# Kernel tuning notes

Hardware: AMD Instinct MI355X
Metric: run time of the kernel (lower is better)

## Reference

```python
import jax, jax.numpy as jnp
import numpy as np

N_NODES = 50000
N_EDGES = 800000
D_FEAT = 96
HOP_NUM = 4


def setup_inputs() -> dict:
    key = jax.random.key(0)
    k1, k2, k3, k4, k5 = jax.random.split(key, 5)
    h = jax.random.normal(k1, (N_NODES, D_FEAT), dtype=jnp.float32)
    # per-node degree-normalization scalar (ndata['d']), e.g. deg^{-1/2}
    d = jax.random.uniform(k2, (N_NODES,), dtype=jnp.float32)
    src = jax.random.randint(k3, (N_EDGES,), 0, N_NODES)
    dst = jax.random.randint(k4, (N_EDGES,), 0, N_NODES)
    # layerRegular: hop_num learned scalars, init U[0,1)
    layer_regular = jax.random.uniform(k5, (HOP_NUM,), dtype=jnp.float32)
    return {"h": h, "d": d, "src": src, "dst": dst, "layer_regular": layer_regular}


def reference(h, d, src, dst, layer_regular):
    # edge weights: e = d_dst * d_src  (edge_applying with m == 1)
    e = (d[dst] * d[src])[:, None]  # [E, 1]

    def spmm(x):
        # update_all(u_mul_e('h','e'), sum): gather src feats, scale, scatter-add to dst
        return jax.ops.segment_sum(x[src] * e, dst, num_segments=N_NODES)

    feat = h
    hops = []
    for i in range(HOP_NUM):
        r = layer_regular[i]
        feat = spmm(feat) * r + (1.0 - r) * feat  # residual blend
        # feature_drop with p=0.0 is identity
        hops.append(feat)
    return jnp.concatenate(hops, axis=1)  # [N, hop_num * D]
```

## Files before the change

### kernel.cpp

```cpp
#include <hip/hip_runtime.h>

#define N_NODES 50000
#define N_EDGES 800000
#define D_FEAT 96
#define HOP_NUM 4
#define OUT_STRIDE (HOP_NUM * D_FEAT)
#define SCAN_B 256
#define NBLK_SCAN ((N_NODES + SCAN_B - 1) / SCAN_B)
#define EB_BLOCKS ((N_EDGES + 255) / 256)
#define F2B_VEC (N_NODES * D_FEAT / 4)
#define F2B_BLOCKS ((F2B_VEC + 255) / 256)

struct Edge { int s; float w; };
typedef float f32x4 __attribute__((ext_vector_type(4)));

__device__ __forceinline__ unsigned short f2bf(float x) {
    union { float f; unsigned u; } c; c.f = x;
    unsigned r = (c.u + 0x7FFFu + ((c.u >> 16) & 1u)) >> 16;
    return (unsigned short)r;
}
__device__ __forceinline__ float bf2f(unsigned short b) {
    union { unsigned u; float f; } c; c.u = ((unsigned)b) << 16;
    return c.f;
}


__global__ void zero_deg_kernel(int* __restrict__ deg) {
    int i = blockIdx.x * blockDim.x + threadIdx.x;
    if (i < N_NODES) deg[i] = 0;
}

__global__ void hist_kernel(const int* __restrict__ dst, int* __restrict__ deg) {
    int e = blockIdx.x * blockDim.x + threadIdx.x;
    if (e >= N_EDGES) return;
    atomicAdd(&deg[dst[e]], 1);
}

__global__ void scanA_kernel(const int* __restrict__ deg, int* __restrict__ off,
                             int* __restrict__ partials, int* __restrict__ cursor) {
    int i = blockIdx.x * SCAN_B + threadIdx.x;
    int v = (i < N_NODES) ? deg[i] : 0;
    int lane = threadIdx.x & 63;
    int wid  = threadIdx.x >> 6;
    int x = v;
    #pragma unroll
    for (int o = 1; o < 64; o <<= 1) {
        int y = __shfl_up(x, o, 64);
        if (lane >= o) x += y;
    }
    __shared__ int wtot[SCAN_B / 64];
    if (lane == 63) wtot[wid] = x;
    __syncthreads();
    int wbase = 0;
    #pragma unroll
    for (int w = 0; w < SCAN_B / 64; ++w) wbase += (w < wid) ? wtot[w] : 0;
    if (i < N_NODES) {
        off[i] = wbase + x - v;
        cursor[i] = 0;
    }
    if (i == N_NODES - 1) off[N_NODES] = wbase + x;
    if (threadIdx.x == SCAN_B - 1) partials[blockIdx.x] = wbase + x;
}

__global__ void scanB_kernel(int* __restrict__ partials) {
    int tid = threadIdx.x;
    int v = (tid < NBLK_SCAN) ? partials[tid] : 0;
    int lane = tid & 63;
    int wid  = tid >> 6;
    int x = v;
    #pragma unroll
    for (int o = 1; o < 64; o <<= 1) {
        int y = __shfl_up(x, o, 64);
        if (lane >= o) x += y;
    }
    __shared__ int wtot[SCAN_B / 64];
    if (lane == 63) wtot[wid] = x;
    __syncthreads();
    int wbase = 0;
    #pragma unroll
    for (int w = 0; w < SCAN_B / 64; ++w) wbase += (w < wid) ? wtot[w] : 0;
    if (tid < NBLK_SCAN) partials[tid] = wbase + x - v;
}

__global__ void scatter_f2bf_kernel(const int* __restrict__ src, const int* __restrict__ dst,
                                    const float* __restrict__ dn,
                                    const int* __restrict__ off, const int* __restrict__ partials,
                                    int* __restrict__ cursor, Edge* __restrict__ edges,
                                    const float* __restrict__ h, unsigned short* __restrict__ tab) {
    int b = blockIdx.x;
    if (b < EB_BLOCKS) {
        int e = b * 256 + threadIdx.x;
        if (e >= N_EDGES) return;
        int t = dst[e];
        int s = src[e];
        float w = dn[s] * dn[t];
        int p = atomicAdd(&cursor[t], 1);
        int idx = off[t] + partials[t >> 8] + p;
        Edge ed; ed.s = s; ed.w = w;
        edges[idx] = ed;
    } else {
        int i = (b - EB_BLOCKS) * 256 + threadIdx.x;
        if (i >= F2B_VEC) return;
        float4 v = ((const float4*)h)[i];
        ushort4 o;
        o.x = f2bf(v.x); o.y = f2bf(v.y); o.z = f2bf(v.z); o.w = f2bf(v.w);
        ((ushort4*)tab)[i] = o;
    }
}

__global__ void spmm_gather_kernel(const unsigned short* __restrict__ tab,
                                   const int* __restrict__ off,
                                   const int* __restrict__ partials,
                                   const Edge* __restrict__ edges,
                                   const float* __restrict__ lr, int hop,
                                   float* __restrict__ out,
                                   unsigned short* __restrict__ tab_next) {
    int gid = (blockIdx.x * blockDim.x + threadIdx.x) >> 5;
    int lane = threadIdx.x & 31;
    if (gid >= N_NODES) return;
    int beg = off[gid] + partials[gid >> 8];
    int end = off[gid + 1] + partials[(gid + 1) >> 8];
    const bool ch = (lane < 24);

    float4 acc = make_float4(0.f, 0.f, 0.f, 0.f);
    for (int b = beg; b < end; b += 32) {
        int m = min(32, end - b);
        int s_l = 0; float w_l = 0.f;
        if (lane < m) {
            Edge ed = edges[b + lane];
            s_l = ed.s; w_l = ed.w;
        }
        int j = 0;
        for (; j + 4 <= m; j += 4) {
            int   s0 = __shfl(s_l, j,     32);
            int   s1 = __shfl(s_l, j + 1, 32);
            int   s2 = __shfl(s_l, j + 2, 32);
            int   s3 = __shfl(s_l, j + 3, 32);
            float w0 = __shfl(w_l, j,     32);
            float w1 = __shfl(w_l, j + 1, 32);
            float w2 = __shfl(w_l, j + 2, 32);
            float w3 = __shfl(w_l, j + 3, 32);
            if (ch) {
                ushort4 u0 = ((const ushort4*)(tab + (long long)s0 * D_FEAT))[lane];
                ushort4 u1 = ((const ushort4*)(tab + (long long)s1 * D_FEAT))[lane];
                ushort4 u2 = ((const ushort4*)(tab + (long long)s2 * D_FEAT))[lane];
                ushort4 u3 = ((const ushort4*)(tab + (long long)s3 * D_FEAT))[lane];
                acc.x = fmaf(bf2f(u0.x), w0, fmaf(bf2f(u1.x), w1, fmaf(bf2f(u2.x), w2, fmaf(bf2f(u3.x), w3, acc.x))));
                acc.y = fmaf(bf2f(u0.y), w0, fmaf(bf2f(u1.y), w1, fmaf(bf2f(u2.y), w2, fmaf(bf2f(u3.y), w3, acc.y))));
                acc.z = fmaf(bf2f(u0.z), w0, fmaf(bf2f(u1.z), w1, fmaf(bf2f(u2.z), w2, fmaf(bf2f(u3.z), w3, acc.z))));
                acc.w = fmaf(bf2f(u0.w), w0, fmaf(bf2f(u1.w), w1, fmaf(bf2f(u2.w), w2, fmaf(bf2f(u3.w), w3, acc.w))));
            }
        }
        for (; j < m; ++j) {
            int   s = __shfl(s_l, j, 32);
            float w = __shfl(w_l, j, 32);
            if (ch) {
                ushort4 u = ((const ushort4*)(tab + (long long)s * D_FEAT))[lane];
                acc.x = fmaf(bf2f(u.x), w, acc.x);
                acc.y = fmaf(bf2f(u.y), w, acc.y);
                acc.z = fmaf(bf2f(u.z), w, acc.z);
                acc.w = fmaf(bf2f(u.w), w, acc.w);
            }
        }
    }

    if (ch) {
        float r = lr[hop];
        ushort4 pu = ((const ushort4*)(tab + (long long)gid * D_FEAT))[lane];
        f32x4 o;
        o.x = acc.x * r + (1.0f - r) * bf2f(pu.x);
        o.y = acc.y * r + (1.0f - r) * bf2f(pu.y);
        o.z = acc.z * r + (1.0f - r) * bf2f(pu.z);
        o.w = acc.w * r + (1.0f - r) * bf2f(pu.w);
        __builtin_nontemporal_store(o, (f32x4*)(out + (long long)gid * OUT_STRIDE) + lane);
        if (tab_next) {
            ushort4 ov;
            ov.x = f2bf(o.x); ov.y = f2bf(o.y); ov.z = f2bf(o.z); ov.w = f2bf(o.w);
            ((ushort4*)(tab_next + (long long)gid * D_FEAT))[lane] = ov;
        }
    }
}

extern "C" void kernel_launch(void* const* d_in, const int* in_sizes, int n_in,
                              void* d_out, int out_size, void* d_ws, size_t ws_size,
                              hipStream_t stream) {
    const float* h   = (const float*)d_in[0];
    const float* dn  = (const float*)d_in[1];
    const int*   src = (const int*)d_in[2];
    const int*   dst = (const int*)d_in[3];
    const float* lr  = (const float*)d_in[4];
    float* out = (float*)d_out;

    char* base = (char*)d_ws;
    Edge* edges = (Edge*)base;                    base += (size_t)N_EDGES * sizeof(Edge);
    unsigned short* tabA = (unsigned short*)base; base += (size_t)N_NODES * D_FEAT * sizeof(unsigned short);
    unsigned short* tabB = (unsigned short*)base; base += (size_t)N_NODES * D_FEAT * sizeof(unsigned short);
    int* off      = (int*)base;                   base += (N_NODES + 1) * sizeof(int);
    int* deg      = (int*)base;                   base += N_NODES * sizeof(int);
    int* cursor   = (int*)base;                   base += N_NODES * sizeof(int);
    int* partials = (int*)base;                   base += NBLK_SCAN * sizeof(int);

    zero_deg_kernel<<<NBLK_SCAN, SCAN_B, 0, stream>>>(deg);
    hist_kernel<<<EB_BLOCKS, 256, 0, stream>>>(dst, deg);
    scanA_kernel<<<NBLK_SCAN, SCAN_B, 0, stream>>>(deg, off, partials, cursor);
    scanB_kernel<<<1, SCAN_B, 0, stream>>>(partials);
    scatter_f2bf_kernel<<<EB_BLOCKS + F2B_BLOCKS, 256, 0, stream>>>(
        src, dst, dn, off, partials, cursor, edges, h, tabA);

    const int GROUPS_PER_BLOCK = 8;
    const int HB = (N_NODES + GROUPS_PER_BLOCK - 1) / GROUPS_PER_BLOCK;
    unsigned short* cur = tabA;
    unsigned short* nxt = tabB;
    for (int hop = 0; hop < HOP_NUM; ++hop) {
        unsigned short* wr = (hop == HOP_NUM - 1) ? (unsigned short*)nullptr : nxt;
        spmm_gather_kernel<<<HB, 256, 0, stream>>>(cur, off, partials, edges, lr, hop,
                                                   out + hop * D_FEAT, wr);
        unsigned short* t = cur; cur = nxt; nxt = t;
    }
}
```

Before: 226.1 us.

## Pack 24-lane node groups densely and drop edge shuffles in SpMM gather

The SpMM gather now gives each node a dense group of 24 threads (192-thread blocks) instead of 32-lane groups with 8 idle lanes. Each thread reads edge records directly, a broadcast load, rather than loading a batch and broadcasting it with shuffles. The fused scatter/bf16-convert launch is split into two kernels, and the output store becomes a normal store instead of a nontemporal one. The aim is to stop wasting a quarter of the lanes and the shuffle overhead. The cost is redundant edge loads per lane, node groups that straddle wavefronts (which can diverge), and one extra launch.

```diff
diff --git a/kernel.cpp b/kernel.cpp
--- a/kernel.cpp
+++ b/kernel.cpp
@@ -9,10 +9,12 @@
 #define NBLK_SCAN ((N_NODES + SCAN_B - 1) / SCAN_B)
 #define EB_BLOCKS ((N_EDGES + 255) / 256)
 #define F2B_VEC (N_NODES * D_FEAT / 4)
-#define F2B_BLOCKS ((F2B_VEC + 255) / 256)
+
+#define GROUP 24
+#define GPB 8
+#define HOP_BLOCK (GROUP * GPB)
 
 struct Edge { int s; float w; };
-typedef float f32x4 __attribute__((ext_vector_type(4)));
 
 __device__ __forceinline__ unsigned short f2bf(float x) {
     union { float f; unsigned u; } c; c.f = x;
@@ -82,102 +84,81 @@
     if (tid < NBLK_SCAN) partials[tid] = wbase + x - v;
 }
 
-__global__ void scatter_f2bf_kernel(const int* __restrict__ src, const int* __restrict__ dst,
-                                    const float* __restrict__ dn,
-                                    const int* __restrict__ off, const int* __restrict__ partials,
-                                    int* __restrict__ cursor, Edge* __restrict__ edges,
-                                    const float* __restrict__ h, unsigned short* __restrict__ tab) {
-    int b = blockIdx.x;
-    if (b < EB_BLOCKS) {
-        int e = b * 256 + threadIdx.x;
-        if (e >= N_EDGES) return;
-        int t = dst[e];
-        int s = src[e];
-        float w = dn[s] * dn[t];
-        int p = atomicAdd(&cursor[t], 1);
-        int idx = off[t] + partials[t >> 8] + p;
-        Edge ed; ed.s = s; ed.w = w;
-        edges[idx] = ed;
-    } else {
-        int i = (b - EB_BLOCKS) * 256 + threadIdx.x;
-        if (i >= F2B_VEC) return;
-        float4 v = ((const float4*)h)[i];
-        ushort4 o;
-        o.x = f2bf(v.x); o.y = f2bf(v.y); o.z = f2bf(v.z); o.w = f2bf(v.w);
-        ((ushort4*)tab)[i] = o;
-    }
-}
-
-__global__ void spmm_gather_kernel(const unsigned short* __restrict__ tab,
-                                   const int* __restrict__ off,
-                                   const int* __restrict__ partials,
-                                   const Edge* __restrict__ edges,
-                                   const float* __restrict__ lr, int hop,
-                                   float* __restrict__ out,
-                                   unsigned short* __restrict__ tab_next) {
-    int gid = (blockIdx.x * blockDim.x + threadIdx.x) >> 5;
-    int lane = threadIdx.x & 31;
+__global__ void scatter_kernel(const int* __restrict__ src, const int* __restrict__ dst,
+                               const float* __restrict__ dn,
+                               const int* __restrict__ off, const int* __restrict__ partials,
+                               int* __restrict__ cursor, Edge* __restrict__ edges) {
+    int e = blockIdx.x * blockDim.x + threadIdx.x;
+    if (e >= N_EDGES) return;
+    int t = dst[e];
+    int s = src[e];
+    float w = dn[s] * dn[t];
+    int p = atomicAdd(&cursor[t], 1);
+    Edge ed; ed.s = s; ed.w = w;
+    edges[off[t] + partials[t >> 8] + p] = ed;
+}
+
+__global__ void f32_to_bf16_kernel(const float* __restrict__ in, unsigned short* __restrict__ out) {
+    int i = blockIdx.x * blockDim.x + threadIdx.x;
+    if (i >= F2B_VEC) return;
+    float4 v = ((const float4*)in)[i];
+    ushort4 o;
+    o.x = f2bf(v.x); o.y = f2bf(v.y); o.z = f2bf(v.z); o.w = f2bf(v.w);
+    ((ushort4*)out)[i] = o;
+}
+
+__global__ void __launch_bounds__(HOP_BLOCK)
+spmm_gather_kernel(const unsigned short* __restrict__ tab,
+                   const int* __restrict__ off,
+                   const int* __restrict__ partials,
+                   const Edge* __restrict__ edges,
+                   const float* __restrict__ lr, int hop,
+                   float* __restrict__ out,
+                   unsigned short* __restrict__ tab_next) {
+    int t = blockIdx.x * HOP_BLOCK + threadIdx.x;
+    int gid = t / GROUP;
+    int lane = t % GROUP;
     if (gid >= N_NODES) return;
     int beg = off[gid] + partials[gid >> 8];
     int end = off[gid + 1] + partials[(gid + 1) >> 8];
-    const bool ch = (lane < 24);
 
     float4 acc = make_float4(0.f, 0.f, 0.f, 0.f);
-    for (int b = beg; b < end; b += 32) {
-        int m = min(32, end - b);
-        int s_l = 0; float w_l = 0.f;
-        if (lane < m) {
-            Edge ed = edges[b + lane];
-            s_l = ed.s; w_l = ed.w;
-        }
-        int j = 0;
-        for (; j + 4 <= m; j += 4) {
-            int   s0 = __shfl(s_l, j,     32);
-            int   s1 = __shfl(s_l, j + 1, 32);
-            int   s2 = __shfl(s_l, j + 2, 32);
-            int   s3 = __shfl(s_l, j + 3, 32);
-            float w0 = __shfl(w_l, j,     32);
-            float w1 = __shfl(w_l, j + 1, 32);
-            float w2 = __shfl(w_l, j + 2, 32);
-            float w3 = __shfl(w_l, j + 3, 32);
-            if (ch) {
-                ushort4 u0 = ((const ushort4*)(tab + (long long)s0 * D_FEAT))[lane];
-                ushort4 u1 = ((const ushort4*)(tab + (long long)s1 * D_FEAT))[lane];
-                ushort4 u2 = ((const ushort4*)(tab + (long long)s2 * D_FEAT))[lane];
-                ushort4 u3 = ((const ushort4*)(tab + (long long)s3 * D_FEAT))[lane];
-                acc.x = fmaf(bf2f(u0.x), w0, fmaf(bf2f(u1.x), w1, fmaf(bf2f(u2.x), w2, fmaf(bf2f(u3.x), w3, acc.x))));
-                acc.y = fmaf(bf2f(u0.y), w0, fmaf(bf2f(u1.y), w1, fmaf(bf2f(u2.y), w2, fmaf(bf2f(u3.y), w3, acc.y))));
-                acc.z = fmaf(bf2f(u0.z), w0, fmaf(bf2f(u1.z), w1, fmaf(bf2f(u2.z), w2, fmaf(bf2f(u3.z), w3, acc.z))));
-                acc.w = fmaf(bf2f(u0.w), w0, fmaf(bf2f(u1.w), w1, fmaf(bf2f(u2.w), w2, fmaf(bf2f(u3.w), w3, acc.w))));
-            }
-        }
-        for (; j < m; ++j) {
-            int   s = __shfl(s_l, j, 32);
-            float w = __shfl(w_l, j, 32);
-            if (ch) {
-                ushort4 u = ((const ushort4*)(tab + (long long)s * D_FEAT))[lane];
-                acc.x = fmaf(bf2f(u.x), w, acc.x);
-                acc.y = fmaf(bf2f(u.y), w, acc.y);
-                acc.z = fmaf(bf2f(u.z), w, acc.z);
-                acc.w = fmaf(bf2f(u.w), w, acc.w);
-            }
-        }
-    }
-
-    if (ch) {
-        float r = lr[hop];
-        ushort4 pu = ((const ushort4*)(tab + (long long)gid * D_FEAT))[lane];
-        f32x4 o;
-        o.x = acc.x * r + (1.0f - r) * bf2f(pu.x);
-        o.y = acc.y * r + (1.0f - r) * bf2f(pu.y);
-        o.z = acc.z * r + (1.0f - r) * bf2f(pu.z);
-        o.w = acc.w * r + (1.0f - r) * bf2f(pu.w);
-        __builtin_nontemporal_store(o, (f32x4*)(out + (long long)gid * OUT_STRIDE) + lane);
-        if (tab_next) {
-            ushort4 ov;
-            ov.x = f2bf(o.x); ov.y = f2bf(o.y); ov.z = f2bf(o.z); ov.w = f2bf(o.w);
-            ((ushort4*)(tab_next + (long long)gid * D_FEAT))[lane] = ov;
-        }
+    int k = beg;
+    for (; k + 4 <= end; k += 4) {
+        Edge e0 = edges[k];
+        Edge e1 = edges[k + 1];
+        Edge e2 = edges[k + 2];
+        Edge e3 = edges[k + 3];
+        ushort4 u0 = ((const ushort4*)(tab + (long long)e0.s * D_FEAT))[lane];
+        ushort4 u1 = ((const ushort4*)(tab + (long long)e1.s * D_FEAT))[lane];
+        ushort4 u2 = ((const ushort4*)(tab + (long long)e2.s * D_FEAT))[lane];
+        ushort4 u3 = ((const ushort4*)(tab + (long long)e3.s * D_FEAT))[lane];
+        acc.x = fmaf(bf2f(u0.x), e0.w, fmaf(bf2f(u1.x), e1.w, fmaf(bf2f(u2.x), e2.w, fmaf(bf2f(u3.x), e3.w, acc.x))));
+        acc.y = fmaf(bf2f(u0.y), e0.w, fmaf(bf2f(u1.y), e1.w, fmaf(bf2f(u2.y), e2.w, fmaf(bf2f(u3.y), e3.w, acc.y))));
+        acc.z = fmaf(bf2f(u0.z), e0.w, fmaf(bf2f(u1.z), e1.w, fmaf(bf2f(u2.z), e2.w, fmaf(bf2f(u3.z), e3.w, acc.z))));
+        acc.w = fmaf(bf2f(u0.w), e0.w, fmaf(bf2f(u1.w), e1.w, fmaf(bf2f(u2.w), e2.w, fmaf(bf2f(u3.w), e3.w, acc.w))));
+    }
+    for (; k < end; ++k) {
+        Edge e = edges[k];
+        ushort4 u = ((const ushort4*)(tab + (long long)e.s * D_FEAT))[lane];
+        acc.x = fmaf(bf2f(u.x), e.w, acc.x);
+        acc.y = fmaf(bf2f(u.y), e.w, acc.y);
+        acc.z = fmaf(bf2f(u.z), e.w, acc.z);
+        acc.w = fmaf(bf2f(u.w), e.w, acc.w);
+    }
+
+    float r = lr[hop];
+    ushort4 pu = ((const ushort4*)(tab + (long long)gid * D_FEAT))[lane];
+    float4 o;
+    o.x = acc.x * r + (1.0f - r) * bf2f(pu.x);
+    o.y = acc.y * r + (1.0f - r) * bf2f(pu.y);
+    o.z = acc.z * r + (1.0f - r) * bf2f(pu.z);
+    o.w = acc.w * r + (1.0f - r) * bf2f(pu.w);
+    ((float4*)(out + (long long)gid * OUT_STRIDE))[lane] = o;
+    if (tab_next) {
+        ushort4 ov;
+        ov.x = f2bf(o.x); ov.y = f2bf(o.y); ov.z = f2bf(o.z); ov.w = f2bf(o.w);
+        ((ushort4*)(tab_next + (long long)gid * D_FEAT))[lane] = ov;
     }
 }
 
@@ -204,17 +185,16 @@
     hist_kernel<<<EB_BLOCKS, 256, 0, stream>>>(dst, deg);
     scanA_kernel<<<NBLK_SCAN, SCAN_B, 0, stream>>>(deg, off, partials, cursor);
     scanB_kernel<<<1, SCAN_B, 0, stream>>>(partials);
-    scatter_f2bf_kernel<<<EB_BLOCKS + F2B_BLOCKS, 256, 0, stream>>>(
-        src, dst, dn, off, partials, cursor, edges, h, tabA);
-
-    const int GROUPS_PER_BLOCK = 8;
-    const int HB = (N_NODES + GROUPS_PER_BLOCK - 1) / GROUPS_PER_BLOCK;
+    scatter_kernel<<<EB_BLOCKS, 256, 0, stream>>>(src, dst, dn, off, partials, cursor, edges);
+    f32_to_bf16_kernel<<<(F2B_VEC + 255) / 256, 256, 0, stream>>>(h, tabA);
+
+    const int HB = (N_NODES + GPB - 1) / GPB;
     unsigned short* cur = tabA;
     unsigned short* nxt = tabB;
     for (int hop = 0; hop < HOP_NUM; ++hop) {
         unsigned short* wr = (hop == HOP_NUM - 1) ? (unsigned short*)nullptr : nxt;
-        spmm_gather_kernel<<<HB, 256, 0, stream>>>(cur, off, partials, edges, lr, hop,
-                                                   out + hop * D_FEAT, wr);
+        spmm_gather_kernel<<<HB, HOP_BLOCK, 0, stream>>>(cur, off, partials, edges, lr, hop,
+                                                         out + hop * D_FEAT, wr);
         unsigned short* t = cur; cur = nxt; nxt = t;
     }
 }
```

Result: slower. 246.1 us (+8.8%).
